# Kernel tuning notes

Measured on AMD Instinct MI355X. Metric: run time of the kernel, lower is better.

## Reference

```python
import jax, jax.numpy as jnp
import numpy as np

B, T, D, H, C = 32, 512, 1024, 1024, 1000


def setup_inputs() -> dict:
    key = jax.random.key(0)
    ks = jax.random.split(key, 12)
    sc = 0.02
    return {
        "features": jax.random.normal(ks[0], (B, T, D), dtype=jnp.float32),
        "Wp": jax.random.normal(ks[1], (H, D), dtype=jnp.float32) * sc,
        "bp": jnp.zeros((H,), jnp.float32),
        "W_ih": jax.random.normal(ks[2], (3 * H, H), dtype=jnp.float32) * sc,
        "b_ih": jnp.zeros((3 * H,), jnp.float32),
        "W_hh": jax.random.normal(ks[3], (3 * H, H), dtype=jnp.float32) * sc,
        "b_hh": jnp.zeros((3 * H,), jnp.float32),
        "W1": jax.random.normal(ks[4], (H, H), dtype=jnp.float32) * sc,
        "b1": jnp.zeros((H,), jnp.float32),
        "W2": jax.random.normal(ks[5], (C, H), dtype=jnp.float32) * sc,
        "b2": jnp.zeros((C,), jnp.float32),
    }


def _gru_scan(gx, W_hh, b_hh):
    # gx: [B, T, 3H] precomputed input-side gate activations
    def step(h, gx_t):
        gh = h @ W_hh.T + b_hh                  # [B, 3H]
        xr, xz, xn = jnp.split(gx_t, 3, axis=-1)
        hr, hz, hn = jnpp if False else jnp.split(gh, 3, axis=-1)
        r = jax.nn.sigmoid(xr + hr)
        z = jax.nn.sigmoid(xz + hz)
        n = jnp.tanh(xn + r * hn)
        h_new = (1.0 - z) * n + z * h
        return h_new, h_new

    h0 = jnp.zeros((gx.shape[0], W_hh.shape[1]), gx.dtype)
    _, hs = jax.lax.scan(step, h0, jnp.swapaxes(gx, 0, 1))  # [T, B, H]
    return jnp.swapaxes(hs, 0, 1)                            # [B, T, H]


def reference(features, Wp, bp, W_ih, b_ih, W_hh, b_hh, W1, b1, W2, b2):
    # pooled inputs: relu(Linear(features))
    x = jax.nn.relu(jnp.einsum("btd,hd->bth", features, Wp) + bp)  # [B,T,H]
    # input-side gate GEMM batched over all timesteps (the recurrence only
    # needs the hidden-side GEMM per step) -- same math as per-step GRUCell
    gx = jnp.einsum("bth,gh->btg", x, W_ih) + b_ih                 # [B,T,3H]
    hs = _gru_scan(gx, W_hh, b_hh)                                  # [B,T,H]
    out = jax.nn.relu(jnp.einsum("bth,oh->bto", hs, W1) + b1)
    out = jnp.einsum("bth,ch->btc", out, W2) + b2                   # [B,T,C]
    return out
```

## Files before the change

kernel.cpp:

```cpp
#include <hip/hip_runtime.h>
#include <hip/hip_bf16.h>
#include <stdint.h>

#define Bb 32
#define Tt 512
#define Dd 1024
#define Hh 1024
#define Cc 1000
#define Mm (Bb*Tt)
#define SENT 0x7F7F7F7Fu

typedef float f32x4 __attribute__((ext_vector_type(4)));
typedef short bf16x8 __attribute__((ext_vector_type(8)));

#define MFMA16(a,b,c) __builtin_amdgcn_mfma_f32_16x16x32_bf16(a,b,c,0,0,0)

static __device__ __forceinline__ unsigned short f2b(float f){
  __hip_bfloat16 h = __float2bfloat16(f);
  union { __hip_bfloat16 h; unsigned short u; } cv; cv.h = h; return cv.u;
}
static __device__ __forceinline__ float b2f(unsigned short u){
  union { unsigned int i; float f; } cv; cv.i = ((unsigned int)u) << 16; return cv.f;
}

static __device__ __forceinline__ void async16(const ushort* g, ushort* l){
  __builtin_amdgcn_global_load_lds((const __attribute__((address_space(1))) unsigned int*)g,
                                   (__attribute__((address_space(3))) unsigned int*)l,
                                   16, 0, 0);
}

template<int FAST>
static __device__ __forceinline__ bf16x8 h_load(const ushort* p){
  bf16x8 r;
  if constexpr (FAST)
    asm volatile("global_load_dwordx4 %0, %1, off sc1" : "=v"(r) : "v"(p) : "memory");
  else
    asm volatile("global_load_dwordx4 %0, %1, off sc0 sc1" : "=v"(r) : "v"(p) : "memory");
  return r;
}
template<int FAST>
static __device__ __forceinline__ void h_store(ushort* p, unsigned int v){
  if constexpr (FAST)
    asm volatile("global_store_dword %0, %1, off sc1" :: "v"(p), "v"(v) : "memory");
  else
    asm volatile("global_store_dword %0, %1, off sc0 sc1" :: "v"(p), "v"(v) : "memory");
}

static __device__ __forceinline__ int load4sys(const int* p){
  int v;
  asm volatile("global_load_dword %0, %1, off sc0 sc1" : "=v"(v) : "v"(p) : "memory");
  asm volatile("s_waitcnt vmcnt(0)" ::: "memory");
  return v;
}
static __device__ __forceinline__ void store4sys(int* p, int v){
  asm volatile("global_store_dword %0, %1, off sc0 sc1" :: "v"(p), "v"(v) : "memory");
}


__global__ void cvt_bf16(const float* __restrict__ in, ushort* __restrict__ out, int n4){
  int i = blockIdx.x*256 + threadIdx.x;
  if (i < n4){
    const float4 v = ((const float4*)in)[i];
    ushort4 o;
    o.x = f2b(v.x); o.y = f2b(v.y); o.z = f2b(v.z); o.w = f2b(v.w);
    ((ushort4*)out)[i] = o;
  }
}

__global__ void pad_w2(const float* __restrict__ w2, const float* __restrict__ b2,
                       ushort* __restrict__ w2p, float* __restrict__ b2p){
  int i = blockIdx.x*256 + threadIdx.x;
  int r = i >> 10, c = i & 1023;
  w2p[i] = (r < Cc) ? f2b(w2[r*1024 + c]) : (ushort)0;
  if (i < 1024) b2p[i] = (i < Cc) ? b2[i] : 0.f;
}


template<int RELU, int OUT_BF16, int PERM_A, int PERM_C>
__global__ __launch_bounds__(256) void gemm_bt(
    const ushort* __restrict__ A, const ushort* __restrict__ Bm,
    const float* __restrict__ bias, void* __restrict__ Cp,
    int M, int N, int K, int ldc, int nout)
{
  __shared__ ushort As[128*32];
  __shared__ ushort Bs[128*32];
  const int tid  = threadIdx.x;
  const int lane = tid & 63;
  const int wave = tid >> 6;
  const int wr = wave >> 1, wc = wave & 1;
  const int r0 = lane & 15, kg = lane >> 4;
  const int m0 = blockIdx.x*128, n0 = blockIdx.y*128;

  const int lrA0 = m0 + (tid>>2);
  const int lrA1 = lrA0 + 64;
  const size_t prA0 = PERM_A ? (size_t)((lrA0 & 511)*32 + (lrA0 >> 9)) : (size_t)lrA0;
  const size_t prA1 = PERM_A ? (size_t)((lrA1 & 511)*32 + (lrA1 >> 9)) : (size_t)lrA1;
  const ushort* aG0 = A  + prA0*K + (tid&3)*8;
  const ushort* aG1 = A  + prA1*K + (tid&3)*8;
  const ushort* bG  = Bm + (size_t)(n0 + (tid>>2))*K + (tid&3)*8;
  ushort* aL = As + tid*8;
  ushort* bL = Bs + tid*8;
  const size_t rstep = (size_t)64*K;

  f32x4 acc[4][4] = {};

  for (int kt = 0; kt < K; kt += 32){
    __syncthreads();
    async16(aG0 + kt, aL);
    async16(aG1 + kt, aL + 2048);
    async16(bG + kt,         bL);
    async16(bG + kt + rstep, bL + 2048);
    __syncthreads();
    bf16x8 af[4], bf_[4];
#pragma unroll
    for (int i=0;i<4;i++) af[i]  = *(const bf16x8*)&As[(wr*64 + i*16 + r0)*32 + kg*8];
#pragma unroll
    for (int j=0;j<4;j++) bf_[j] = *(const bf16x8*)&Bs[(wc*64 + j*16 + r0)*32 + kg*8];
#pragma unroll
    for (int i=0;i<4;i++)
#pragma unroll
      for (int j=0;j<4;j++)
        acc[i][j] = MFMA16(af[i], bf_[j], acc[i][j]);
  }

  const int rowb = m0 + wr*64 + kg*4;
  const int colb = n0 + wc*64 + r0;
#pragma unroll
  for (int i=0;i<4;i++){
#pragma unroll
    for (int j=0;j<4;j++){
      const int c = colb + j*16;
      if (c >= nout) continue;
      const float bv = bias ? bias[c] : 0.f;
#pragma unroll
      for (int q=0;q<4;q++){
        const int r = rowb + i*16 + q;
        const size_t pr = PERM_C ? (size_t)((r & 511)*32 + (r >> 9)) : (size_t)r;
        float v = acc[i][j][q] + bv;
        if (RELU) v = fmaxf(v, 0.f);
        if (OUT_BF16) ((ushort*)Cp)[pr*ldc + c] = f2b(v);
        else          ((float* )Cp)[pr*ldc + c] = v;
      }
    }
  }
}


template<int FAST>
static __device__ __forceinline__ void scan_body(
    const int g, const int m, const int tid,
    const ushort* __restrict__ Whh, const float* __restrict__ bhh,
    const ushort* __restrict__ gxT, ushort* __restrict__ hsAll,
    float* __restrict__ red)
{
  const int wave = tid >> 6;
  const int lane = tid & 63;
  const int r0 = lane & 15, kg = lane >> 4;
  const int kbase = wave*128 + kg*8;

  bf16x8 wb[6][4];
#pragma unroll
  for (int n=0;n<6;n++){
    const ushort* wr_ = Whh + ((size_t)((n>>1)*1024 + m*32 + (n&1)*16 + r0))*1024 + kbase;
#pragma unroll
    for (int ks=0;ks<4;ks++)
      wb[n][ks] = *(const bf16x8*)(wr_ + ks*32);
  }

  const int eb = tid >> 4;
  const int eu = (tid & 15)*2;
  const int jg = m*32 + eu;
  float br0=0,br1=0,bz0=0,bz1=0,bn0=0,bn1=0;
  if (tid < 64){
    br0 = bhh[jg];       br1 = bhh[jg+1];
    bz0 = bhh[1024+jg];  bz1 = bhh[1024+jg+1];
    bn0 = bhh[2048+jg];  bn1 = bhh[2048+jg+1];
  }
  float hold0 = 0.f, hold1 = 0.f;

  for (int t = 0; t < Tt; ++t){
#pragma unroll
    for (int n=0;n<6;n++)
#pragma unroll
      for (int ks=0;ks<4;ks++)
        asm volatile("" : "+v"(wb[n][ks]));

    unsigned xr=0, xz=0, xn=0;
    if (tid < 64){
      const ushort* gb = gxT + (size_t)(t*32 + g*4 + eb)*3072 + jg;
      xr = *(const unsigned*)(gb);
      xz = *(const unsigned*)(gb + 1024);
      xn = *(const unsigned*)(gb + 2048);
    }

    const ushort* aB = hsAll + (size_t)(t*32 + g*4 + (r0 & 3))*1024 + kbase;
    bf16x8 ha[4];
    int again;
    do {
#pragma unroll
      for (int ks=0;ks<4;ks++) ha[ks] = h_load<FAST>(aB + ks*32);
      asm volatile("s_waitcnt vmcnt(0)" ::: "memory");
      __builtin_amdgcn_sched_barrier(0);
      unsigned sent = 0;
#pragma unroll
      for (int ks=0;ks<4;ks++){
        union { bf16x8 v; unsigned u[4]; } A; A.v = ha[ks];
#pragma unroll
        for (int q=0;q<4;q++) sent |= (A.u[q] == SENT);
      }
      again = __any((int)sent);
    } while (again);

    f32x4 acc[6] = {};
#pragma unroll
    for (int ks=0;ks<4;ks++)
#pragma unroll
      for (int n=0;n<6;n++)
        acc[n] = MFMA16(ha[ks], wb[n][ks], acc[n]);

#pragma unroll
    for (int n=0;n<6;n++)
      *(f32x4*)&red[(wave*6 + n)*256 + lane*4] = acc[n];
    __syncthreads();

    if (tid < 64){
      float rs0=0,zs0=0,ns0=0, rs1=0,zs1=0,ns1=0;
#pragma unroll
      for (int w=0;w<8;w++){
        int j;
        j = eu;      rs0 += red[(w*6 + (j>>4))*256 + (j&15)*4 + eb];
        j = eu+1;    rs1 += red[(w*6 + (j>>4))*256 + (j&15)*4 + eb];
        j = 32+eu;   zs0 += red[(w*6 + (j>>4))*256 + (j&15)*4 + eb];
        j = 33+eu;   zs1 += red[(w*6 + (j>>4))*256 + (j&15)*4 + eb];
        j = 64+eu;   ns0 += red[(w*6 + (j>>4))*256 + (j&15)*4 + eb];
        j = 65+eu;   ns1 += red[(w*6 + (j>>4))*256 + (j&15)*4 + eb];
      }
      float h0, h1;
      {
        const float r = 1.f/(1.f + expf(-(b2f((ushort)(xr & 0xffff)) + rs0 + br0)));
        const float z = 1.f/(1.f + expf(-(b2f((ushort)(xz & 0xffff)) + zs0 + bz0)));
        const float n = tanhf(b2f((ushort)(xn & 0xffff)) + r*(ns0 + bn0));
        h0 = (1.f - z)*n + z*hold0; hold0 = h0;
      }
      {
        const float r = 1.f/(1.f + expf(-(b2f((ushort)(xr >> 16)) + rs1 + br1)));
        const float z = 1.f/(1.f + expf(-(b2f((ushort)(xz >> 16)) + zs1 + bz1)));
        const float n = tanhf(b2f((ushort)(xn >> 16)) + r*(ns1 + bn1));
        h1 = (1.f - z)*n + z*hold1; hold1 = h1;
      }
      const unsigned packed = (unsigned)f2b(h0) | ((unsigned)f2b(h1) << 16);
      h_store<FAST>(hsAll + (size_t)((t+1)*32 + g*4 + eb)*1024 + jg, packed);
    }
    __syncthreads();
  }
}

__global__ __launch_bounds__(512, 1) void gru_scan(
    const ushort* __restrict__ Whh, const float* __restrict__ bhh,
    const ushort* __restrict__ gxT,
    ushort* __restrict__ hsAll,
    int* __restrict__ xccTab)
{
  __shared__ float red[8*6*256];
  __shared__ int fastFlag;
  const int bid = blockIdx.x;
  const int g = bid & 7, m = bid >> 3;
  const int tid = threadIdx.x;
  int* decTab = xccTab + 256;

  if (tid == 0){
    int myxcc;
    asm volatile("s_getreg_b32 %0, hwreg(HW_REG_XCC_ID)" : "=s"(myxcc));
    store4sys(&xccTab[bid], myxcc);
    if (m == 0){
      int ok = 1;
      long budget = 200000;
      for (int p = 0; p < 32 && ok; ++p){
        int v;
        do {
          v = load4sys(&xccTab[p*8 + g]);
          if (v == -1){ __builtin_amdgcn_s_sleep(1); if (--budget <= 0){ ok = 0; break; } }
        } while (v == -1);
        if (v != myxcc) ok = 0;
      }
      store4sys(&decTab[g], ok);
      fastFlag = ok;
    } else {
      int v;
      do {
        v = load4sys(&decTab[g]);
        if (v == -1) __builtin_amdgcn_s_sleep(1);
      } while (v == -1);
      fastFlag = v;
    }
  }
  __syncthreads();

  if (fastFlag) scan_body<1>(g, m, tid, Whh, bhh, gxT, hsAll, red);
  else          scan_body<0>(g, m, tid, Whh, bhh, gxT, hsAll, red);
}


extern "C" void kernel_launch(void* const* d_in, const int* in_sizes, int n_in,
                              void* d_out, int out_size, void* d_ws, size_t ws_size,
                              hipStream_t stream)
{
  const float* features = (const float*)d_in[0];
  const float* Wp  = (const float*)d_in[1];
  const float* bp  = (const float*)d_in[2];
  const float* Wih = (const float*)d_in[3];
  const float* bih = (const float*)d_in[4];
  const float* Whh = (const float*)d_in[5];
  const float* bhh = (const float*)d_in[6];
  const float* W1  = (const float*)d_in[7];
  const float* b1  = (const float*)d_in[8];
  const float* W2  = (const float*)d_in[9];
  const float* b2  = (const float*)d_in[10];
  float* out = (float*)d_out;

  char* w = (char*)d_ws;
  auto alloc = [&](size_t bytes){ char* p = w; w += (bytes + 255) & ~(size_t)255; return p; };
  ushort* fb    = (ushort*)alloc((size_t)Mm*Dd*2);
  ushort* xb    = (ushort*)alloc((size_t)Mm*Hh*2);
  ushort* gxT   = (ushort*)alloc((size_t)Mm*3*Hh*2);
  ushort* hsAll = (ushort*)alloc((size_t)(Tt+1)*Bb*Hh*2);
  ushort* o1    = (ushort*)alloc((size_t)Mm*Hh*2);
  ushort* wpb   = (ushort*)alloc((size_t)Hh*Dd*2);
  ushort* wihb  = (ushort*)alloc((size_t)3*Hh*Hh*2);
  ushort* whhb  = (ushort*)alloc((size_t)3*Hh*Hh*2);
  ushort* w1b   = (ushort*)alloc((size_t)Hh*Hh*2);
  ushort* w2b   = (ushort*)alloc((size_t)1024*Hh*2);
  float*  b2p   = (float*)alloc(1024*4);
  int*    xccTab= (int*)alloc(264*4);
  ushort* hsT   = hsAll + (size_t)Bb*Hh;

  hipMemsetAsync(hsAll, 0x7F, (size_t)(Tt+1)*Bb*Hh*2, stream);
  hipMemsetAsync(hsAll, 0x00, (size_t)Bb*Hh*2, stream);
  hipMemsetAsync(xccTab, 0xFF, 264*4, stream);

  auto cvt = [&](const float* src, ushort* dst, size_t n){
    int n4 = (int)(n/4);
    hipLaunchKernelGGL(cvt_bf16, dim3((n4+255)/256), dim3(256), 0, stream, src, dst, n4);
  };
  cvt(features, fb, (size_t)Mm*Dd);
  cvt(Wp,  wpb,  (size_t)Hh*Dd);
  cvt(Wih, wihb, (size_t)3*Hh*Hh);
  cvt(Whh, whhb, (size_t)3*Hh*Hh);
  cvt(W1,  w1b,  (size_t)Hh*Hh);
  hipLaunchKernelGGL(pad_w2, dim3((1024*1024)/256), dim3(256), 0, stream, W2, b2, w2b, b2p);

  hipLaunchKernelGGL((gemm_bt<1,1,0,0>), dim3(Mm/128, Hh/128), dim3(256), 0, stream,
                     fb, wpb, bp, (void*)xb, Mm, Hh, Dd, Hh, Hh);
  hipLaunchKernelGGL((gemm_bt<0,1,0,1>), dim3(Mm/128, (3*Hh)/128), dim3(256), 0, stream,
                     xb, wihb, bih, (void*)gxT, Mm, 3*Hh, Hh, 3*Hh, 3*Hh);

  hipLaunchKernelGGL(gru_scan, dim3(256), dim3(512), 0, stream,
                     whhb, bhh, gxT, hsAll, xccTab);

  hipLaunchKernelGGL((gemm_bt<1,1,1,0>), dim3(Mm/128, Hh/128), dim3(256), 0, stream,
                     hsT, w1b, b1, (void*)o1, Mm, Hh, Hh, Hh, Hh);
  hipLaunchKernelGGL((gemm_bt<0,0,0,0>), dim3(Mm/128, 1024/128), dim3(256), 0, stream,
                     o1, w2b, b2p, (void*)out, Mm, 1024, Hh, Cc, Cc);
}
```

Baseline: 1.968 ms.

## Replace sentinel polling with per-block step flags and double-buffered reduction in GRU scan

The cross-block handoff of the hidden state no longer polls the data itself for a sentinel value. Each block now publishes a per-step counter flag, and each wave polls the four flags of the producer blocks it depends on before loading h. The reduction buffer in LDS is double-buffered so the second __syncthreads per step can be dropped. The next step's gx values are prefetched, and expf/tanhf are replaced with fast __expf-based forms. This also removes the large sentinel memset of hsAll. The risks are memory-ordering subtleties between the flag and the data, and some loss of accuracy in the gate maths.

```diff
diff --git a/kernel.cpp b/kernel.cpp
--- a/kernel.cpp
+++ b/kernel.cpp
@@ -8,10 +8,10 @@
 #define Hh 1024
 #define Cc 1000
 #define Mm (Bb*Tt)
-#define SENT 0x7F7F7F7Fu
 
 typedef float f32x4 __attribute__((ext_vector_type(4)));
 typedef short bf16x8 __attribute__((ext_vector_type(8)));
+typedef int   i32x4  __attribute__((ext_vector_type(4)));
 
 #define MFMA16(a,b,c) __builtin_amdgcn_mfma_f32_16x16x32_bf16(a,b,c,0,0,0)
 
@@ -40,6 +40,22 @@
 }
 template<int FAST>
 static __device__ __forceinline__ void h_store(ushort* p, unsigned int v){
+  if constexpr (FAST)
+    asm volatile("global_store_dword %0, %1, off sc1" :: "v"(p), "v"(v) : "memory");
+  else
+    asm volatile("global_store_dword %0, %1, off sc0 sc1" :: "v"(p), "v"(v) : "memory");
+}
+template<int FAST>
+static __device__ __forceinline__ i32x4 flag_load4(const int* p){
+  i32x4 r;
+  if constexpr (FAST)
+    asm volatile("global_load_dwordx4 %0, %1, off sc1" : "=v"(r) : "v"(p) : "memory");
+  else
+    asm volatile("global_load_dwordx4 %0, %1, off sc0 sc1" : "=v"(r) : "v"(p) : "memory");
+  return r;
+}
+template<int FAST>
+static __device__ __forceinline__ void flag_store(int* p, int v){
   if constexpr (FAST)
     asm volatile("global_store_dword %0, %1, off sc1" :: "v"(p), "v"(v) : "memory");
   else
@@ -151,7 +167,7 @@
     const int g, const int m, const int tid,
     const ushort* __restrict__ Whh, const float* __restrict__ bhh,
     const ushort* __restrict__ gxT, ushort* __restrict__ hsAll,
-    float* __restrict__ red)
+    int* __restrict__ flags, float* __restrict__ red)
 {
   const int wave = tid >> 6;
   const int lane = tid & 63;
@@ -164,12 +180,13 @@
     const ushort* wr_ = Whh + ((size_t)((n>>1)*1024 + m*32 + (n&1)*16 + r0))*1024 + kbase;
 #pragma unroll
     for (int ks=0;ks<4;ks++)
-      wb[n][ks] = *(const bf16x8*)(wr_ + ks*32);
-  }
+      asm volatile("global_load_dwordx4 %0, %1, off" : "=v"(wb[n][ks]) : "v"(wr_ + ks*32));
+  }
+  asm volatile("s_waitcnt vmcnt(0)" ::: "memory");
 
   const int eb = tid >> 4;
-  const int eu = (tid & 15)*2;
-  const int jg = m*32 + eu;
+  const int u0 = (tid & 15)*2;
+  const int jg = m*32 + u0;
   float br0=0,br1=0,bz0=0,bz1=0,bn0=0,bn1=0;
   if (tid < 64){
     br0 = bhh[jg];       br1 = bhh[jg+1];
@@ -178,38 +195,42 @@
   }
   float hold0 = 0.f, hold1 = 0.f;
 
+  unsigned xr=0, xz=0, xn=0, xrN=0, xzN=0, xnN=0;
+  if (tid < 64){
+    const ushort* gb = gxT + (size_t)(g*4 + eb)*3072 + jg;
+    asm volatile("global_load_dword %0, %1, off" : "=v"(xr) : "v"(gb));
+    asm volatile("global_load_dword %0, %1, off" : "=v"(xz) : "v"(gb + 1024));
+    asm volatile("global_load_dword %0, %1, off" : "=v"(xn) : "v"(gb + 2048));
+  }
+
+  int* myflag = &flags[g*32 + m];
+  const int* fl = &flags[g*32 + wave*4];
+
   for (int t = 0; t < Tt; ++t){
-#pragma unroll
-    for (int n=0;n<6;n++)
-#pragma unroll
-      for (int ks=0;ks<4;ks++)
-        asm volatile("" : "+v"(wb[n][ks]));
-
-    unsigned xr=0, xz=0, xn=0;
-    if (tid < 64){
-      const ushort* gb = gxT + (size_t)(t*32 + g*4 + eb)*3072 + jg;
-      xr = *(const unsigned*)(gb);
-      xz = *(const unsigned*)(gb + 1024);
-      xn = *(const unsigned*)(gb + 2048);
+    const int buf = t & 1;
+
+    for (;;){
+      i32x4 f = flag_load4<FAST>(fl);
+      asm volatile("s_waitcnt vmcnt(0)" ::: "memory");
+      if (f[0] >= t && f[1] >= t && f[2] >= t && f[3] >= t) break;
     }
 
     const ushort* aB = hsAll + (size_t)(t*32 + g*4 + (r0 & 3))*1024 + kbase;
     bf16x8 ha[4];
-    int again;
-    do {
-#pragma unroll
-      for (int ks=0;ks<4;ks++) ha[ks] = h_load<FAST>(aB + ks*32);
+#pragma unroll
+    for (int ks=0;ks<4;ks++) ha[ks] = h_load<FAST>(aB + ks*32);
+
+    if (tid < 64){
+      const int tn = (t+1 < Tt) ? t+1 : t;
+      const ushort* gb = gxT + (size_t)(tn*32 + g*4 + eb)*3072 + jg;
+      asm volatile("global_load_dword %0, %1, off" : "=v"(xrN) : "v"(gb));
+      asm volatile("global_load_dword %0, %1, off" : "=v"(xzN) : "v"(gb + 1024));
+      asm volatile("global_load_dword %0, %1, off" : "=v"(xnN) : "v"(gb + 2048));
+      asm volatile("s_waitcnt vmcnt(3)" ::: "memory");
+    } else {
       asm volatile("s_waitcnt vmcnt(0)" ::: "memory");
-      __builtin_amdgcn_sched_barrier(0);
-      unsigned sent = 0;
-#pragma unroll
-      for (int ks=0;ks<4;ks++){
-        union { bf16x8 v; unsigned u[4]; } A; A.v = ha[ks];
-#pragma unroll
-        for (int q=0;q<4;q++) sent |= (A.u[q] == SENT);
-      }
-      again = __any((int)sent);
-    } while (again);
+    }
+    __builtin_amdgcn_sched_barrier(0);
 
     f32x4 acc[6] = {};
 #pragma unroll
@@ -220,38 +241,45 @@
 
 #pragma unroll
     for (int n=0;n<6;n++)
-      *(f32x4*)&red[(wave*6 + n)*256 + lane*4] = acc[n];
+      *(f32x4*)&red[buf*12288 + (wave*6 + n)*256 + lane*4] = acc[n];
     __syncthreads();
 
     if (tid < 64){
       float rs0=0,zs0=0,ns0=0, rs1=0,zs1=0,ns1=0;
+      const float* rb = red + buf*12288;
 #pragma unroll
       for (int w=0;w<8;w++){
         int j;
-        j = eu;      rs0 += red[(w*6 + (j>>4))*256 + (j&15)*4 + eb];
-        j = eu+1;    rs1 += red[(w*6 + (j>>4))*256 + (j&15)*4 + eb];
-        j = 32+eu;   zs0 += red[(w*6 + (j>>4))*256 + (j&15)*4 + eb];
-        j = 33+eu;   zs1 += red[(w*6 + (j>>4))*256 + (j&15)*4 + eb];
-        j = 64+eu;   ns0 += red[(w*6 + (j>>4))*256 + (j&15)*4 + eb];
-        j = 65+eu;   ns1 += red[(w*6 + (j>>4))*256 + (j&15)*4 + eb];
+        j = u0;      rs0 += rb[(w*6 + (j>>4))*256 + (j&15)*4 + eb];
+        j = u0+1;    rs1 += rb[(w*6 + (j>>4))*256 + (j&15)*4 + eb];
+        j = 32+u0;   zs0 += rb[(w*6 + (j>>4))*256 + (j&15)*4 + eb];
+        j = 33+u0;   zs1 += rb[(w*6 + (j>>4))*256 + (j&15)*4 + eb];
+        j = 64+u0;   ns0 += rb[(w*6 + (j>>4))*256 + (j&15)*4 + eb];
+        j = 65+u0;   ns1 += rb[(w*6 + (j>>4))*256 + (j&15)*4 + eb];
       }
       float h0, h1;
       {
-        const float r = 1.f/(1.f + expf(-(b2f((ushort)(xr & 0xffff)) + rs0 + br0)));
-        const float z = 1.f/(1.f + expf(-(b2f((ushort)(xz & 0xffff)) + zs0 + bz0)));
-        const float n = tanhf(b2f((ushort)(xn & 0xffff)) + r*(ns0 + bn0));
+        const float r = 1.f/(1.f + __expf(-(b2f((ushort)(xr & 0xffff)) + rs0 + br0)));
+        const float z = 1.f/(1.f + __expf(-(b2f((ushort)(xz & 0xffff)) + zs0 + bz0)));
+        const float a = b2f((ushort)(xn & 0xffff)) + r*(ns0 + bn0);
+        const float e = __expf(-2.f*a);
+        const float n = (1.f - e)/(1.f + e);
         h0 = (1.f - z)*n + z*hold0; hold0 = h0;
       }
       {
-        const float r = 1.f/(1.f + expf(-(b2f((ushort)(xr >> 16)) + rs1 + br1)));
-        const float z = 1.f/(1.f + expf(-(b2f((ushort)(xz >> 16)) + zs1 + bz1)));
-        const float n = tanhf(b2f((ushort)(xn >> 16)) + r*(ns1 + bn1));
+        const float r = 1.f/(1.f + __expf(-(b2f((ushort)(xr >> 16)) + rs1 + br1)));
+        const float z = 1.f/(1.f + __expf(-(b2f((ushort)(xz >> 16)) + zs1 + bz1)));
+        const float a = b2f((ushort)(xn >> 16)) + r*(ns1 + bn1);
+        const float e = __expf(-2.f*a);
+        const float n = (1.f - e)/(1.f + e);
         h1 = (1.f - z)*n + z*hold1; hold1 = h1;
       }
       const unsigned packed = (unsigned)f2b(h0) | ((unsigned)f2b(h1) << 16);
       h_store<FAST>(hsAll + (size_t)((t+1)*32 + g*4 + eb)*1024 + jg, packed);
-    }
-    __syncthreads();
+      asm volatile("s_waitcnt vmcnt(0)" ::: "memory");
+      if (tid == 0) flag_store<FAST>(myflag, t+1);
+    }
+    xr = xrN; xz = xzN; xn = xnN;
   }
 }
 
@@ -259,9 +287,10 @@
     const ushort* __restrict__ Whh, const float* __restrict__ bhh,
     const ushort* __restrict__ gxT,
     ushort* __restrict__ hsAll,
+    int* __restrict__ flags,
     int* __restrict__ xccTab)
 {
-  __shared__ float red[8*6*256];
+  __shared__ float red[2*12288];
   __shared__ int fastFlag;
   const int bid = blockIdx.x;
   const int g = bid & 7, m = bid >> 3;
@@ -296,8 +325,8 @@
   }
   __syncthreads();
 
-  if (fastFlag) scan_body<1>(g, m, tid, Whh, bhh, gxT, hsAll, red);
-  else          scan_body<0>(g, m, tid, Whh, bhh, gxT, hsAll, red);
+  if (fastFlag) scan_body<1>(g, m, tid, Whh, bhh, gxT, hsAll, flags, red);
+  else          scan_body<0>(g, m, tid, Whh, bhh, gxT, hsAll, flags, red);
 }
 
 
@@ -331,11 +360,12 @@
   ushort* w1b   = (ushort*)alloc((size_t)Hh*Hh*2);
   ushort* w2b   = (ushort*)alloc((size_t)1024*Hh*2);
   float*  b2p   = (float*)alloc(1024*4);
+  int*    flags = (int*)alloc(256*4);
   int*    xccTab= (int*)alloc(264*4);
   ushort* hsT   = hsAll + (size_t)Bb*Hh;
 
-  hipMemsetAsync(hsAll, 0x7F, (size_t)(Tt+1)*Bb*Hh*2, stream);
   hipMemsetAsync(hsAll, 0x00, (size_t)Bb*Hh*2, stream);
+  hipMemsetAsync(flags, 0x00, 256*4, stream);
   hipMemsetAsync(xccTab, 0xFF, 264*4, stream);
 
   auto cvt = [&](const float* src, ushort* dst, size_t n){
@@ -355,7 +385,7 @@
                      xb, wihb, bih, (void*)gxT, Mm, 3*Hh, Hh, 3*Hh, 3*Hh);
 
   hipLaunchKernelGGL(gru_scan, dim3(256), dim3(512), 0, stream,
-                     whhb, bhh, gxT, hsAll, xccTab);
+                     whhb, bhh, gxT, hsAll, flags, xccTab);
 
   hipLaunchKernelGGL((gemm_bt<1,1,1,0>), dim3(Mm/128, Hh/128), dim3(256), 0, stream,
                      hsT, w1b, b1, (void*)o1, Mm, Hh, Hh, Hh, Hh);
```

After: 3.980 ms. 2.02x slower.

## Prefetch next-step gate inputs, double-buffer reduction LDS, use fast exp

Applied to the files above, without the earlier changes.

The GRU recurrence now prefetches the next timestep's input-side gate values with inline-asm global loads issued during the current step's MFMA work. The per-step LDS reduction buffer is double-buffered so the trailing barrier can be removed, leaving one __syncthreads per timestep. Sigmoid and tanh now use __expf-based formulas instead of expf/tanhf, which shortens the elementwise tail at some cost in accuracy. The prefetched registers are copied without an explicit vmcnt wait, which relies on compiler and hardware ordering and risks reading a load that has not yet arrived.

```diff
diff --git a/kernel.cpp b/kernel.cpp
--- a/kernel.cpp
+++ b/kernel.cpp
@@ -168,8 +168,8 @@
   }
 
   const int eb = tid >> 4;
-  const int eu = (tid & 15)*2;
-  const int jg = m*32 + eu;
+  const int u0 = (tid & 15)*2;
+  const int jg = m*32 + u0;
   float br0=0,br1=0,bz0=0,bz1=0,bn0=0,bn1=0;
   if (tid < 64){
     br0 = bhh[jg];       br1 = bhh[jg+1];
@@ -178,20 +178,22 @@
   }
   float hold0 = 0.f, hold1 = 0.f;
 
+  unsigned xr=0, xz=0, xn=0, xrN=0, xzN=0, xnN=0;
+  if (tid < 64){
+    const ushort* gb = gxT + (size_t)(g*4 + eb)*3072 + jg;
+    asm volatile("global_load_dword %0, %1, off" : "=v"(xr) : "v"(gb));
+    asm volatile("global_load_dword %0, %1, off" : "=v"(xz) : "v"(gb + 1024));
+    asm volatile("global_load_dword %0, %1, off" : "=v"(xn) : "v"(gb + 2048));
+  }
+
   for (int t = 0; t < Tt; ++t){
+    const int buf = t & 1;
+
 #pragma unroll
     for (int n=0;n<6;n++)
 #pragma unroll
       for (int ks=0;ks<4;ks++)
         asm volatile("" : "+v"(wb[n][ks]));
-
-    unsigned xr=0, xz=0, xn=0;
-    if (tid < 64){
-      const ushort* gb = gxT + (size_t)(t*32 + g*4 + eb)*3072 + jg;
-      xr = *(const unsigned*)(gb);
-      xz = *(const unsigned*)(gb + 1024);
-      xn = *(const unsigned*)(gb + 2048);
-    }
 
     const ushort* aB = hsAll + (size_t)(t*32 + g*4 + (r0 & 3))*1024 + kbase;
     bf16x8 ha[4];
@@ -211,6 +213,13 @@
       again = __any((int)sent);
     } while (again);
 
+    if (tid < 64 && t+1 < Tt){
+      const ushort* gb = gxT + (size_t)((t+1)*32 + g*4 + eb)*3072 + jg;
+      asm volatile("global_load_dword %0, %1, off" : "=v"(xrN) : "v"(gb));
+      asm volatile("global_load_dword %0, %1, off" : "=v"(xzN) : "v"(gb + 1024));
+      asm volatile("global_load_dword %0, %1, off" : "=v"(xnN) : "v"(gb + 2048));
+    }
+
     f32x4 acc[6] = {};
 #pragma unroll
     for (int ks=0;ks<4;ks++)
@@ -220,38 +229,43 @@
 
 #pragma unroll
     for (int n=0;n<6;n++)
-      *(f32x4*)&red[(wave*6 + n)*256 + lane*4] = acc[n];
+      *(f32x4*)&red[buf*12288 + (wave*6 + n)*256 + lane*4] = acc[n];
     __syncthreads();
 
     if (tid < 64){
       float rs0=0,zs0=0,ns0=0, rs1=0,zs1=0,ns1=0;
+      const float* rb = red + buf*12288;
 #pragma unroll
       for (int w=0;w<8;w++){
         int j;
-        j = eu;      rs0 += red[(w*6 + (j>>4))*256 + (j&15)*4 + eb];
-        j = eu+1;    rs1 += red[(w*6 + (j>>4))*256 + (j&15)*4 + eb];
-        j = 32+eu;   zs0 += red[(w*6 + (j>>4))*256 + (j&15)*4 + eb];
-        j = 33+eu;   zs1 += red[(w*6 + (j>>4))*256 + (j&15)*4 + eb];
-        j = 64+eu;   ns0 += red[(w*6 + (j>>4))*256 + (j&15)*4 + eb];
-        j = 65+eu;   ns1 += red[(w*6 + (j>>4))*256 + (j&15)*4 + eb];
+        j = u0;      rs0 += rb[(w*6 + (j>>4))*256 + (j&15)*4 + eb];
+        j = u0+1;    rs1 += rb[(w*6 + (j>>4))*256 + (j&15)*4 + eb];
+        j = 32+u0;   zs0 += rb[(w*6 + (j>>4))*256 + (j&15)*4 + eb];
+        j = 33+u0;   zs1 += rb[(w*6 + (j>>4))*256 + (j&15)*4 + eb];
+        j = 64+u0;   ns0 += rb[(w*6 + (j>>4))*256 + (j&15)*4 + eb];
+        j = 65+u0;   ns1 += rb[(w*6 + (j>>4))*256 + (j&15)*4 + eb];
       }
       float h0, h1;
       {
-        const float r = 1.f/(1.f + expf(-(b2f((ushort)(xr & 0xffff)) + rs0 + br0)));
-        const float z = 1.f/(1.f + expf(-(b2f((ushort)(xz & 0xffff)) + zs0 + bz0)));
-        const float n = tanhf(b2f((ushort)(xn & 0xffff)) + r*(ns0 + bn0));
+        const float r = 1.f/(1.f + __expf(-(b2f((ushort)(xr & 0xffff)) + rs0 + br0)));
+        const float z = 1.f/(1.f + __expf(-(b2f((ushort)(xz & 0xffff)) + zs0 + bz0)));
+        const float a = b2f((ushort)(xn & 0xffff)) + r*(ns0 + bn0);
+        const float e = __expf(-2.f*a);
+        const float n = (1.f - e)/(1.f + e);
         h0 = (1.f - z)*n + z*hold0; hold0 = h0;
       }
       {
-        const float r = 1.f/(1.f + expf(-(b2f((ushort)(xr >> 16)) + rs1 + br1)));
-        const float z = 1.f/(1.f + expf(-(b2f((ushort)(xz >> 16)) + zs1 + bz1)));
-        const float n = tanhf(b2f((ushort)(xn >> 16)) + r*(ns1 + bn1));
+        const float r = 1.f/(1.f + __expf(-(b2f((ushort)(xr >> 16)) + rs1 + br1)));
+        const float z = 1.f/(1.f + __expf(-(b2f((ushort)(xz >> 16)) + zs1 + bz1)));
+        const float a = b2f((ushort)(xn >> 16)) + r*(ns1 + bn1);
+        const float e = __expf(-2.f*a);
+        const float n = (1.f - e)/(1.f + e);
         h1 = (1.f - z)*n + z*hold1; hold1 = h1;
       }
       const unsigned packed = (unsigned)f2b(h0) | ((unsigned)f2b(h1) << 16);
       h_store<FAST>(hsAll + (size_t)((t+1)*32 + g*4 + eb)*1024 + jg, packed);
+      xr = xrN; xz = xzN; xn = xnN;
     }
-    __syncthreads();
   }
 }
 
@@ -261,7 +275,7 @@
     ushort* __restrict__ hsAll,
     int* __restrict__ xccTab)
 {
-  __shared__ float red[8*6*256];
+  __shared__ float red[2*12288];
   __shared__ int fastFlag;
   const int bid = blockIdx.x;
   const int g = bid & 7, m = bid >> 3;
```

Result: faster. 1.890 ms (-4.0%).
